# Optimization experiments

Measured on AMD Instinct MI355X. Metric: run time of the kernel, lower is better.

Reference implementation:

```python
import jax, jax.numpy as jnp
import numpy as np

N, S, D, H, L = 1024, 128, 128, 4, 2  # nodes, seq_len, d_model(=heads*C), heads, layers
C = D // H
EPS = 1e-5


def _bn(x, g, b):
    # torch BatchNorm1d training mode applied to [N, D, S]: per-channel stats over (node, seq)
    m = x.mean(axis=(0, 1))
    v = x.var(axis=(0, 1))  # biased variance, matching torch BN normalization
    return (x - m) * jax.lax.rsqrt(v + EPS) * g + b


def _ln(x, g, b):
    m = x.mean(-1, keepdims=True)
    v = x.var(-1, keepdims=True)
    return (x - m) * jax.lax.rsqrt(v + EPS) * g + b


def setup_inputs() -> dict:
    key = jax.random.key(0)
    ks = jax.random.split(key, 16)
    w = lambda k, shape: (jax.random.normal(k, shape, jnp.float32) * 0.05)
    x = jax.random.normal(ks[0], (N, S, D), jnp.float32)
    pad_mask = (jax.random.uniform(ks[1], (N, S, S)) > 0.2).astype(jnp.float32)
    ones = lambda shape: jnp.ones(shape, jnp.float32)
    zeros = lambda shape: jnp.zeros(shape, jnp.float32)
    inp = {
        'x': x, 'pad_mask': pad_mask,
        'lin_in_W': w(ks[2], (D, D)), 'lin_in_b': zeros((D,)),
        'in_bn_g': ones((D,)), 'in_bn_b': zeros((D,)),
        'q_W': w(ks[3], (L, D, D)), 'q_b': zeros((L, D)),
        'q_bn_g': ones((L, D)), 'q_bn_b': zeros((L, D)),
        'k_W': w(ks[4], (L, D, D)), 'k_b': zeros((L, D)),
        'k_bn_g': ones((L, D)), 'k_bn_b': zeros((L, D)),
        'v_W': w(ks[5], (L, D, D)), 'v_b': zeros((L, D)),
        'v_bn_g': ones((L, D)), 'v_bn_b': zeros((L, D)),
        'ln_g': ones((L, D)), 'ln_b': zeros((L, D)),
        'ff_W': w(ks[6], (L, D, D)), 'ff_b': zeros((L, D)),
        'ff_bn_g': ones((L, D)), 'ff_bn_b': zeros((L, D)),
        'skip_W': w(ks[7], (L, D, D)), 'skip_b': zeros((L, D)),
        'skip_bn_g': ones((L, D)), 'skip_bn_b': zeros((L, D)),
    }
    return inp


def reference(x, pad_mask, lin_in_W, lin_in_b, in_bn_g, in_bn_b,
              q_W, q_b, q_bn_g, q_bn_b, k_W, k_b, k_bn_g, k_bn_b,
              v_W, v_b, v_bn_g, v_bn_b, ln_g, ln_b,
              ff_W, ff_b, ff_bn_g, ff_bn_b, skip_W, skip_b, skip_bn_g, skip_bn_b):
    # DetourTransformer.forward: lin_in -> in_bn -> L DetourTransformerLayers -> take seq position 0
    h = _bn(x @ lin_in_W.T + lin_in_b, in_bn_g, in_bn_b)
    mask = pad_mask[:, None]  # [N,1,S,S], multiplicative mask applied BEFORE softmax
    for l in range(L):
        q = _bn(h @ q_W[l].T + q_b[l], q_bn_g[l], q_bn_b[l]).reshape(N, S, H, C)
        k = _bn(h @ k_W[l].T + k_b[l], k_bn_g[l], k_bn_b[l]).reshape(N, S, H, C)
        v = _bn(h @ v_W[l].T + v_b[l], v_bn_g[l], v_bn_b[l]).reshape(N, S, H, C)
        alpha = jnp.einsum('nshc,nthc->nhst', q, k) * mask  # no 1/sqrt(C) scaling in source
        attn = jax.nn.softmax(alpha, axis=-1)
        agg = jnp.einsum('nhst,nthc->nshc', attn, v).reshape(N, S, D)  # concat=True
        out = _ln(agg + h, ln_g[l], ln_b[l])
        ff = _bn(out @ ff_W[l].T + ff_b[l], ff_bn_g[l], ff_bn_b[l])
        out = _ln(out + ff, ln_g[l], ln_b[l])  # same shared LayerNorm params reused
        x_r = _bn(h @ skip_W[l].T + skip_b[l], skip_bn_g[l], skip_bn_b[l])
        h = out + x_r  # root_weight=True, beta=False
    return h[:, 0]
```

## Files before the change

kernel.cpp:

```cpp
#include <hip/hip_runtime.h>
#include <hip/hip_bf16.h>


typedef __attribute__((ext_vector_type(8))) short short8v;
typedef __attribute__((ext_vector_type(16))) float f32x16;

#define NBATCH 1024
#define SEQ    128
#define DIM    128
#define NLAYER 2
#define MTOT   (NBATCH*SEQ)
#define EPSF   1e-5f
#define INV_M  (1.0f/131072.0f)
#define HM32   ((long)MTOT * 32)
#define WMAT   16384

__device__ __forceinline__ float bf2f(ushort s) {
  return __uint_as_float(((uint)s) << 16);
}
__device__ __forceinline__ ushort f2bf(float f) {
  uint u = __float_as_uint(f);
  return (ushort)((u + 0x7FFFu + ((u >> 16) & 1u)) >> 16);
}
__device__ __forceinline__ void bfsplit(float x, short& h, short& l) {
  ushort hu = f2bf(x);
  h = (short)hu;
  l = (short)f2bf(x - bf2f(hu));
}

struct WPtrs { const float* p[11]; };

__global__ __launch_bounds__(256) void prep_w(
    WPtrs wp, ushort* __restrict__ dhi, ushort* __restrict__ dlo)
{
  const int gid = blockIdx.x * 256 + threadIdx.x;
  const int m = gid >> 11;
  const int rem = gid & 2047;
  const int j = rem >> 4, kc = rem & 15;
  const float* src = wp.p[m];
  float4 a = *(const float4*)(src + j * DIM + kc * 8);
  float4 b = *(const float4*)(src + j * DIM + kc * 8 + 4);
  float xs[8] = {a.x, a.y, a.z, a.w, b.x, b.y, b.z, b.w};
  short8v vh, vl;
#pragma unroll
  for (int i = 0; i < 8; ++i) { short h, l; bfsplit(xs[i], h, l); vh[i] = h; vl[i] = l; }
  const int nt = j >> 5, ln = j & 31;
  const int idx = m * WMAT + kc * 1024 + nt * 256 + ln * 8;
  *(short8v*)(dhi + idx) = vh;
  *(short8v*)(dlo + idx) = vl;
}

__global__ __launch_bounds__(256) void pack_mask(
    const float* __restrict__ mask, uint4* __restrict__ mb)
{
  const int lane = threadIdx.x & 63;
  const int wv   = (blockIdx.x * 256 + threadIdx.x) >> 6;
  const int NW   = gridDim.x * 4;
  for (int row = wv; row < MTOT; row += NW) {
    const float a = mask[(long)row * SEQ + lane];
    const float b = mask[(long)row * SEQ + 64 + lane];
    const unsigned long long lo = __ballot(a != 0.f);
    const unsigned long long hi = __ballot(b != 0.f);
    if (lane == 0) {
      uint4 w;
      w.x = (uint)lo; w.y = (uint)(lo >> 32);
      w.z = (uint)hi; w.w = (uint)(hi >> 32);
      mb[row] = w;
    }
  }
}

template<int OM>
__global__ __launch_bounds__(256) void gemm_one(
    const float* __restrict__ A,
    const ushort* __restrict__ Whi, const ushort* __restrict__ Wlo,
    void* __restrict__ outp, float* __restrict__ stats)
{
  __shared__ ushort Wh[16384];
  __shared__ ushort Wl[16384];
  __shared__ float tb[4][512];
  const int tid = threadIdx.x;
  const int lane = tid & 63, wid = tid >> 6;
  const int hi = lane >> 5, ln = lane & 31;
  const long m0 = (long)blockIdx.x * 128;
  const long arow = m0 + wid * 32 + ln;

#pragma unroll
  for (int i = 0; i < 8; ++i) {
    ((short8v*)Wh)[i * 256 + tid] = ((const short8v*)Whi)[i * 256 + tid];
    ((short8v*)Wl)[i * 256 + tid] = ((const short8v*)Wlo)[i * 256 + tid];
  }

  short8v ahi[8], alo[8];
  {
    const float* ar = A + arow * DIM + hi * 8;
#pragma unroll
    for (int kt = 0; kt < 8; ++kt) {
      float4 a0 = *(const float4*)(ar + kt * 16);
      float4 a1 = *(const float4*)(ar + kt * 16 + 4);
      float xs[8] = {a0.x, a0.y, a0.z, a0.w, a1.x, a1.y, a1.z, a1.w};
      short8v vh, vl;
#pragma unroll
      for (int i = 0; i < 8; ++i) { short h, l; bfsplit(xs[i], h, l); vh[i] = h; vl[i] = l; }
      ahi[kt] = vh; alo[kt] = vl;
    }
  }
  __syncthreads();

  f32x16 acc[4];
#pragma unroll
  for (int nt = 0; nt < 4; ++nt)
#pragma unroll
    for (int r = 0; r < 16; ++r) acc[nt][r] = 0.f;

#pragma unroll
  for (int kt = 0; kt < 8; ++kt) {
    const int co = (kt * 2 + hi) * 1024 + ln * 8;
#pragma unroll
    for (int nt = 0; nt < 4; ++nt) {
      short8v bh = *(const short8v*)(Wh + co + nt * 256);
      short8v bl = *(const short8v*)(Wl + co + nt * 256);
      acc[nt] = __builtin_amdgcn_mfma_f32_32x32x16_bf16(ahi[kt], bh, acc[nt], 0, 0, 0);
      acc[nt] = __builtin_amdgcn_mfma_f32_32x32x16_bf16(alo[kt], bh, acc[nt], 0, 0, 0);
      acc[nt] = __builtin_amdgcn_mfma_f32_32x32x16_bf16(ahi[kt], bl, acc[nt], 0, 0, 0);
    }
  }

  float ps[4], pq[4];
#pragma unroll
  for (int nt = 0; nt < 4; ++nt) { ps[nt] = 0.f; pq[nt] = 0.f; }

  if constexpr (OM == 0) {
#pragma unroll
    for (int nt = 0; nt < 4; ++nt) {
#pragma unroll
      for (int h2 = 0; h2 < 2; ++h2) {
#pragma unroll
        for (int rr = 0; rr < 8; ++rr) {
          const int r = h2 * 8 + rr;
          const float v = acc[nt][r];
          ps[nt] += v; pq[nt] += v * v;
          const int lrow = (rr & 3) + 8 * (rr >> 2) + 4 * hi;
          tb[wid][lrow * 32 + ln] = v;
        }
#pragma unroll
        for (int i = 0; i < 2; ++i) {
          const int lrow = i * 8 + (lane >> 3);
          float4 v = *(const float4*)&tb[wid][lrow * 32 + (lane & 7) * 4];
          *(float4*)((float*)outp + (m0 + wid * 32 + h2 * 16 + lrow) * DIM + nt * 32 + (lane & 7) * 4) = v;
        }
      }
    }
  } else {
    ushort* utb = (ushort*)&tb[wid][0];
#pragma unroll
    for (int nt = 0; nt < 4; ++nt) {
#pragma unroll
      for (int r = 0; r < 16; ++r) {
        const float v = acc[nt][r];
        ps[nt] += v; pq[nt] += v * v;
        const int row = (r & 3) + 8 * (r >> 2) + 4 * hi;
        utb[row * 32 + ln] = f2bf(v);
      }
      ushort* dst = (ushort*)outp + (long)nt * HM32 + (m0 + wid * 32) * 32;
      short8v v0 = *(const short8v*)&utb[lane * 8];
      short8v v1 = *(const short8v*)&utb[512 + lane * 8];
      *(short8v*)(dst + lane * 8)       = v0;
      *(short8v*)(dst + 512 + lane * 8) = v1;
    }
  }

#pragma unroll
  for (int nt = 0; nt < 4; ++nt) {
    ps[nt] += __shfl_xor(ps[nt], 32);
    pq[nt] += __shfl_xor(pq[nt], 32);
  }
  float* cs = (float*)tb;
  __syncthreads();
  if (tid < 256) cs[tid] = 0.f;
  __syncthreads();
  if (hi == 0) {
#pragma unroll
    for (int nt = 0; nt < 4; ++nt) {
      atomicAdd(&cs[nt * 32 + ln], ps[nt]);
      atomicAdd(&cs[128 + nt * 32 + ln], pq[nt]);
    }
  }
  __syncthreads();
  if (tid < 128) {
    atomicAdd(&stats[tid],       cs[tid]);
    atomicAdd(&stats[128 + tid], cs[128 + tid]);
  }
}

__global__ __launch_bounds__(256) void gemm_qkvs(
    const float* __restrict__ A,
    const ushort* __restrict__ whi, const ushort* __restrict__ wlo,
    ushort* __restrict__ o0, ushort* __restrict__ o1,
    ushort* __restrict__ o2, ushort* __restrict__ o3,
    float* __restrict__ st0, float* __restrict__ st1,
    float* __restrict__ st2, float* __restrict__ st3)
{
  __shared__ ushort wbuf[2][16384];
  __shared__ ushort qtb[4][1024];
  __shared__ float cs2[1024];
  const int tid = threadIdx.x;
  const int lane = tid & 63, wid = tid >> 6;
  const int hi = lane >> 5, ln = lane & 31;
  const long m0 = (long)blockIdx.x * 128;
  const long arow = m0 + wid * 32 + ln;

  short8v ahi[8], alo[8];
  {
    const float* ar = A + arow * DIM + hi * 8;
#pragma unroll
    for (int kt = 0; kt < 8; ++kt) {
      float4 a0 = *(const float4*)(ar + kt * 16);
      float4 a1 = *(const float4*)(ar + kt * 16 + 4);
      float xs[8] = {a0.x, a0.y, a0.z, a0.w, a1.x, a1.y, a1.z, a1.w};
      short8v vh, vl;
#pragma unroll
      for (int i = 0; i < 8; ++i) { short h, l; bfsplit(xs[i], h, l); vh[i] = h; vl[i] = l; }
      ahi[kt] = vh; alo[kt] = vl;
    }
  }

  {
    const short8v* sh = (const short8v*)(whi);
    const short8v* sl = (const short8v*)(wlo);
    short8v* d = (short8v*)wbuf[0];
#pragma unroll
    for (int i = 0; i < 4; ++i) d[i * 256 + tid] = sh[i * 256 + tid];
#pragma unroll
    for (int i = 0; i < 4; ++i) d[1024 + i * 256 + tid] = sl[i * 256 + tid];
    cs2[tid] = 0.f; cs2[256 + tid] = 0.f; cs2[512 + tid] = 0.f; cs2[768 + tid] = 0.f;
  }

  f32x16 acc[4];
  __syncthreads();

#pragma unroll
  for (int s = 0; s < 8; ++s) {
    const int w = s >> 1, half = s & 1;
    constexpr int wofl[4] = {0, 1, 2, 4};

    short8v nw[8];
    if (s < 7) {
      const int ns = s + 1;
      const int off = wofl[ns >> 1] * WMAT + (ns & 1) * 8192;
      const short8v* sh = (const short8v*)(whi + off);
      const short8v* sl = (const short8v*)(wlo + off);
#pragma unroll
      for (int i = 0; i < 4; ++i) nw[i] = sh[i * 256 + tid];
#pragma unroll
      for (int i = 0; i < 4; ++i) nw[4 + i] = sl[i * 256 + tid];
    }

    if (half == 0) {
#pragma unroll
      for (int nt = 0; nt < 4; ++nt)
#pragma unroll
        for (int r = 0; r < 16; ++r) acc[nt][r] = 0.f;
    }

    const ushort* wt = wbuf[s & 1];
#pragma unroll
    for (int ktl = 0; ktl < 4; ++ktl) {
      const int kt = half * 4 + ktl;
      const int co = (ktl * 2 + hi) * 1024 + ln * 8;
#pragma unroll
      for (int nt = 0; nt < 4; ++nt) {
        short8v bh = *(const short8v*)(wt + co + nt * 256);
        short8v bl = *(const short8v*)(wt + 8192 + co + nt * 256);
        acc[nt] = __builtin_amdgcn_mfma_f32_32x32x16_bf16(ahi[kt], bh, acc[nt], 0, 0, 0);
        acc[nt] = __builtin_amdgcn_mfma_f32_32x32x16_bf16(alo[kt], bh, acc[nt], 0, 0, 0);
        acc[nt] = __builtin_amdgcn_mfma_f32_32x32x16_bf16(ahi[kt], bl, acc[nt], 0, 0, 0);
      }
    }

    if (s < 7) {
      short8v* d = (short8v*)wbuf[(s + 1) & 1];
#pragma unroll
      for (int i = 0; i < 4; ++i) d[i * 256 + tid] = nw[i];
#pragma unroll
      for (int i = 0; i < 4; ++i) d[1024 + i * 256 + tid] = nw[4 + i];
    }

    if (half == 1) {
      ushort* outp = (w == 0) ? o0 : (w == 1) ? o1 : (w == 2) ? o2 : o3;
      float lps[4], lpq[4];
#pragma unroll
      for (int nt = 0; nt < 4; ++nt) { lps[nt] = 0.f; lpq[nt] = 0.f; }
#pragma unroll
      for (int nt = 0; nt < 4; ++nt) {
#pragma unroll
        for (int r = 0; r < 16; ++r) {
          const float v = acc[nt][r];
          lps[nt] += v; lpq[nt] += v * v;
          const int row = (r & 3) + 8 * (r >> 2) + 4 * hi;
          qtb[wid][row * 32 + ln] = f2bf(v);
        }
        ushort* dst = outp + (long)nt * HM32 + (m0 + wid * 32) * 32;
        short8v v0 = *(const short8v*)&qtb[wid][lane * 8];
        short8v v1 = *(const short8v*)&qtb[wid][512 + lane * 8];
        *(short8v*)(dst + lane * 8)       = v0;
        *(short8v*)(dst + 512 + lane * 8) = v1;
      }
#pragma unroll
      for (int nt = 0; nt < 4; ++nt) {
        lps[nt] += __shfl_xor(lps[nt], 32);
        lpq[nt] += __shfl_xor(lpq[nt], 32);
      }
      if (hi == 0) {
#pragma unroll
        for (int nt = 0; nt < 4; ++nt) {
          atomicAdd(&cs2[w * 256 + nt * 32 + ln], lps[nt]);
          atomicAdd(&cs2[w * 256 + 128 + nt * 32 + ln], lpq[nt]);
        }
      }
    }
    __syncthreads();
  }

  if (tid < 128) {
    atomicAdd(&st0[tid],       cs2[tid]);
    atomicAdd(&st0[128 + tid], cs2[128 + tid]);
    atomicAdd(&st1[tid],       cs2[256 + tid]);
    atomicAdd(&st1[128 + tid], cs2[384 + tid]);
    atomicAdd(&st2[tid],       cs2[512 + tid]);
    atomicAdd(&st2[128 + tid], cs2[640 + tid]);
    atomicAdd(&st3[tid],       cs2[768 + tid]);
    atomicAdd(&st3[128 + tid], cs2[896 + tid]);
  }
}

__global__ __launch_bounds__(256) void bn_apply(
    float* __restrict__ x, const float* __restrict__ st,
    const float* __restrict__ g, const float* __restrict__ b)
{
  __shared__ float sc[128], bi[128];
  const int tid = threadIdx.x;
  if (tid < 128) {
    float mean = st[tid] * INV_M;
    float var  = st[128 + tid] * INV_M - mean * mean;
    float s = rsqrtf(var + EPSF) * g[tid];
    sc[tid] = s;
    bi[tid] = b[tid] - mean * s;
  }
  __syncthreads();
  const long total4 = (long)MTOT * DIM / 4;
  for (long i = (long)blockIdx.x * 256 + tid; i < total4; i += (long)gridDim.x * 256) {
    float4 vv = ((const float4*)x)[i];
    const int c = (int)((i * 4) & 127);
    vv.x = vv.x * sc[c + 0] + bi[c + 0];
    vv.y = vv.y * sc[c + 1] + bi[c + 1];
    vv.z = vv.z * sc[c + 2] + bi[c + 2];
    vv.w = vv.w * sc[c + 3] + bi[c + 3];
    ((float4*)x)[i] = vv;
  }
}

__global__ __launch_bounds__(256) void attn_ln(
    const ushort* __restrict__ q, const ushort* __restrict__ k_in,
    const ushort* __restrict__ v_in,
    float* hbuf,
    const uint4* __restrict__ mb,
    const float* __restrict__ qst, const float* __restrict__ kst, const float* __restrict__ vst,
    const float* __restrict__ qg, const float* __restrict__ qbb,
    const float* __restrict__ kg, const float* __restrict__ kbb,
    const float* __restrict__ vg, const float* __restrict__ vbb,
    const float* __restrict__ lng, const float* __restrict__ lnb)
{
  __shared__ ushort Vp[128 * 136];
  __shared__ float qsc[128], qbi[128], ksc[128], kbi[128];
  __shared__ float reds[32][4], redq[32][4];
  __shared__ float2 rmv[32];

  const int tid = threadIdx.x;
  const int lane = tid & 63, hh = tid >> 6;
  const int hi = lane >> 5, ln = lane & 31;
  const int n = blockIdx.x;
  const long nb = (long)n * SEQ;
  const long hbase = (long)hh * HM32 + nb * 32;

  if (tid < 128) {
    const int c = tid;
    float m, v, s;
    m = qst[c] * INV_M; v = qst[128 + c] * INV_M - m * m;
    s = rsqrtf(v + EPSF) * qg[c];  qsc[c] = s; qbi[c] = qbb[c] - m * s;
    m = kst[c] * INV_M; v = kst[128 + c] * INV_M - m * m;
    s = rsqrtf(v + EPSF) * kg[c];  ksc[c] = s; kbi[c] = kbb[c] - m * s;
  }
  const int cg = hh * 32 + ln;
  float vs, vb0;
  {
    float m = vst[cg] * INV_M;
    float v = vst[128 + cg] * INV_M - m * m;
    vs = rsqrtf(v + EPSF) * vg[cg];
    vb0 = vbb[cg] - m * vs;
  }
  const float lgc = lng[cg], lbc = lnb[cg];

#pragma unroll
  for (int it = 0; it < 8; ++it) {
    const int t = it * 16 + (lane >> 2);
    const int c0 = (lane & 3) * 8;
    short8v vv = *(const short8v*)(v_in + hbase + (long)t * 32 + c0);
    const int tl = t & 31;
    const int kt = tl >> 4;
    const int rem = tl & 15;
    const int slot = (t & 96) + (kt << 4) + ((rem >> 2) & 1) * 8 + ((rem & 3) | (((rem >> 3) & 1) << 2));
#pragma unroll
    for (int i = 0; i < 8; ++i) Vp[(hh * 32 + c0 + i) * 136 + slot] = (ushort)vv[i];
  }
  __syncthreads();

  short8v kfr[4][2];
#pragma unroll
  for (int nt = 0; nt < 4; ++nt)
#pragma unroll
    for (int kt = 0; kt < 2; ++kt) {
      short8v raw = *(const short8v*)(k_in + hbase + (long)(nt * 32 + ln) * 32 + kt * 16 + hi * 8);
      short8v f;
#pragma unroll
      for (int i = 0; i < 8; ++i) {
        const int c = hh * 32 + kt * 16 + hi * 8 + i;
        f[i] = (short)f2bf(bf2f((ushort)raw[i]) * ksc[c] + kbi[c]);
      }
      kfr[nt][kt] = f;
    }

  for (int mt = 0; mt < 4; ++mt) {
    short8v qfr[2];
#pragma unroll
    for (int kt = 0; kt < 2; ++kt) {
      short8v raw = *(const short8v*)(q + hbase + (long)(mt * 32 + ln) * 32 + kt * 16 + hi * 8);
      short8v f;
#pragma unroll
      for (int i = 0; i < 8; ++i) {
        const int c = hh * 32 + kt * 16 + hi * 8 + i;
        f[i] = (short)f2bf(bf2f((ushort)raw[i]) * qsc[c] + qbi[c]);
      }
      qfr[kt] = f;
    }

    f32x16 st[4];
#pragma unroll
    for (int nt = 0; nt < 4; ++nt)
#pragma unroll
      for (int r = 0; r < 16; ++r) st[nt][r] = 0.f;
#pragma unroll
    for (int nt = 0; nt < 4; ++nt) {
      st[nt] = __builtin_amdgcn_mfma_f32_32x32x16_bf16(kfr[nt][0], qfr[0], st[nt], 0, 0, 0);
      st[nt] = __builtin_amdgcn_mfma_f32_32x32x16_bf16(kfr[nt][1], qfr[1], st[nt], 0, 0, 0);
    }

    const uint4 bw = mb[nb + mt * 32 + ln];
    float mx = -1e30f;
#pragma unroll
    for (int nt = 0; nt < 4; ++nt) {
      const uint word = (nt == 0) ? bw.x : (nt == 1) ? bw.y : (nt == 2) ? bw.z : bw.w;
#pragma unroll
      for (int r = 0; r < 16; ++r) {
        const int crow = (r & 3) + 8 * (r >> 2) + 4 * hi;
        st[nt][r] = ((word >> crow) & 1u) ? st[nt][r] : 0.f;
        mx = fmaxf(mx, st[nt][r]);
      }
    }
    mx = fmaxf(mx, __shfl_xor(mx, 32));
    float sum = 0.f;
#pragma unroll
    for (int nt = 0; nt < 4; ++nt)
#pragma unroll
      for (int r = 0; r < 16; ++r) {
        const float e = __expf(st[nt][r] - mx);
        st[nt][r] = e;
        sum += e;
      }
    sum += __shfl_xor(sum, 32);
    const float inv = 1.f / sum;

    f32x16 o;
#pragma unroll
    for (int r = 0; r < 16; ++r) o[r] = 0.f;
#pragma unroll
    for (int nt = 0; nt < 4; ++nt) {
#pragma unroll
      for (int kt = 0; kt < 2; ++kt) {
        short8v phi, plo;
#pragma unroll
        for (int j = 0; j < 8; ++j) {
          short h, l; bfsplit(st[nt][kt * 8 + j] * inv, h, l);
          phi[j] = h; plo[j] = l;
        }
        short8v vb = *(const short8v*)&Vp[(long)cg * 136 + nt * 32 + kt * 16 + hi * 8];
        o = __builtin_amdgcn_mfma_f32_32x32x16_bf16(phi, vb, o, 0, 0, 0);
        o = __builtin_amdgcn_mfma_f32_32x32x16_bf16(plo, vb, o, 0, 0, 0);
      }
    }

    float yv[16];
#pragma unroll
    for (int r = 0; r < 16; ++r) {
      const int sl = (r & 3) + 8 * (r >> 2) + 4 * hi;
      const float hval = hbuf[(nb + mt * 32 + sl) * DIM + cg];
      yv[r] = vs * o[r] + vb0 + hval;
    }

#pragma unroll
    for (int r = 0; r < 16; ++r) {
      float s = yv[r], q2 = yv[r] * yv[r];
      s += __shfl_xor(s, 1);  q2 += __shfl_xor(q2, 1);
      s += __shfl_xor(s, 2);  q2 += __shfl_xor(q2, 2);
      s += __shfl_xor(s, 4);  q2 += __shfl_xor(q2, 4);
      s += __shfl_xor(s, 8);  q2 += __shfl_xor(q2, 8);
      s += __shfl_xor(s, 16); q2 += __shfl_xor(q2, 16);
      if (ln == 0) {
        const int sl = (r & 3) + 8 * (r >> 2) + 4 * hi;
        reds[sl][hh] = s; redq[sl][hh] = q2;
      }
    }
    __syncthreads();
    if (tid < 32) {
      const float s  = reds[tid][0] + reds[tid][1] + reds[tid][2] + reds[tid][3];
      const float q2 = redq[tid][0] + redq[tid][1] + redq[tid][2] + redq[tid][3];
      const float mean = s * (1.f / 128.f);
      const float var  = q2 * (1.f / 128.f) - mean * mean;
      rmv[tid] = make_float2(mean, rsqrtf(var + EPSF));
    }
    __syncthreads();
#pragma unroll
    for (int r = 0; r < 16; ++r) {
      const int sl = (r & 3) + 8 * (r >> 2) + 4 * hi;
      const float2 mr = rmv[sl];
      hbuf[(nb + mt * 32 + sl) * DIM + cg] = (yv[r] - mr.x) * mr.y * lgc + lbc;
    }
  }
}

template <bool FINAL>
__global__ __launch_bounds__(256) void fuse2_k(
    const float* t1, const ushort* __restrict__ ffr, const ushort* __restrict__ skr,
    const float* __restrict__ fst, const float* __restrict__ sst,
    const float* __restrict__ fg, const float* __restrict__ fb,
    const float* __restrict__ sg, const float* __restrict__ sb,
    const float* __restrict__ lg, const float* __restrict__ lb,
    float* out)
{
  const int lane = threadIdx.x & 63;
  const int c = lane * 2;
  float fs0, fbias0, fs1, fbias1, ss0, sbias0, ss1, sbias1;
  {
    float m0 = fst[c] * INV_M;
    float v0 = fst[128 + c] * INV_M - m0 * m0;
    fs0 = rsqrtf(v0 + EPSF) * fg[c];       fbias0 = fb[c] - m0 * fs0;
    float m1 = fst[c + 1] * INV_M;
    float v1 = fst[128 + c + 1] * INV_M - m1 * m1;
    fs1 = rsqrtf(v1 + EPSF) * fg[c + 1];   fbias1 = fb[c + 1] - m1 * fs1;
    float n0 = sst[c] * INV_M;
    float w0 = sst[128 + c] * INV_M - n0 * n0;
    ss0 = rsqrtf(w0 + EPSF) * sg[c];       sbias0 = sb[c] - n0 * ss0;
    float n1 = sst[c + 1] * INV_M;
    float w1 = sst[128 + c + 1] * INV_M - n1 * n1;
    ss1 = rsqrtf(w1 + EPSF) * sg[c + 1];   sbias1 = sb[c + 1] - n1 * ss1;
  }
  const float lg0 = lg[c], lg1 = lg[c + 1], lb0 = lb[c], lb1 = lb[c + 1];
  const int wid = (blockIdx.x * 256 + threadIdx.x) >> 6;
  const int NW  = gridDim.x * 4;
  const int ROWS = FINAL ? NBATCH : MTOT;
  const long thm = (long)(c >> 5) * HM32;
  for (int r = wid; r < ROWS; r += NW) {
    const long m   = FINAL ? (long)r * SEQ : (long)r;
    const long off = m * DIM + c;
    const long hm  = thm + m * 32 + (c & 31);
    float2 tv = *(const float2*)(t1 + off);
    uint fv = *(const uint*)(ffr + hm);
    uint sv = *(const uint*)(skr + hm);
    float f0 = bf2f((ushort)(fv & 0xFFFFu)), f1 = bf2f((ushort)(fv >> 16));
    float s0 = bf2f((ushort)(sv & 0xFFFFu)), s1 = bf2f((ushort)(sv >> 16));
    float y0 = tv.x + f0 * fs0 + fbias0;
    float y1 = tv.y + f1 * fs1 + fbias1;
    float s = y0 + y1, sq = y0 * y0 + y1 * y1;
#pragma unroll
    for (int o = 32; o; o >>= 1) { s += __shfl_xor(s, o); sq += __shfl_xor(sq, o); }
    const float mean = s * (1.f / 128.f);
    const float var  = sq * (1.f / 128.f) - mean * mean;
    const float rs   = rsqrtf(var + EPSF);
    float o0 = (y0 - mean) * rs * lg0 + lb0 + (s0 * ss0 + sbias0);
    float o1 = (y1 - mean) * rs * lg1 + lb1 + (s1 * ss1 + sbias1);
    const long ooff = FINAL ? ((long)r * DIM + c) : off;
    *(float2*)(out + ooff) = make_float2(o0, o1);
  }
}

extern "C" void kernel_launch(void* const* d_in, const int* in_sizes, int n_in,
                              void* d_out, int out_size, void* d_ws, size_t ws_size,
                              hipStream_t stream)
{
  (void)in_sizes; (void)n_in; (void)out_size; (void)ws_size;
  const float* x    = (const float*)d_in[0];
  const float* mask = (const float*)d_in[1];
  const float* linW = (const float*)d_in[2];
  const float* ing  = (const float*)d_in[4];
  const float* inb  = (const float*)d_in[5];
  const float* qW   = (const float*)d_in[6];
  const float* qg   = (const float*)d_in[8];
  const float* qb   = (const float*)d_in[9];
  const float* kW   = (const float*)d_in[10];
  const float* kg   = (const float*)d_in[12];
  const float* kb   = (const float*)d_in[13];
  const float* vW   = (const float*)d_in[14];
  const float* vg   = (const float*)d_in[16];
  const float* vb   = (const float*)d_in[17];
  const float* lng  = (const float*)d_in[18];
  const float* lnb  = (const float*)d_in[19];
  const float* ffW  = (const float*)d_in[20];
  const float* ffg  = (const float*)d_in[22];
  const float* ffb  = (const float*)d_in[23];
  const float* skW  = (const float*)d_in[24];
  const float* skg  = (const float*)d_in[26];
  const float* skb  = (const float*)d_in[27];

  const long MD = (long)MTOT * DIM;
  float*  stats = (float*)d_ws;
  ushort* whi   = (ushort*)((char*)d_ws + 16384);
  ushort* wlo   = whi + 11 * WMAT;
  float*  h     = (float*)(wlo + 11 * WMAT);
  ushort* qbuf  = (ushort*)(h + MD);
  ushort* kbuf  = qbuf + MD;
  ushort* vbuf  = kbuf + MD;
  ushort* sbuf  = vbuf + MD;
  uint4*  mbits = (uint4*)(sbuf + MD);
  ushort* ffbuf = qbuf;

  hipMemsetAsync(stats, 0, 11 * 256 * sizeof(float), stream);

  WPtrs wp;
  wp.p[0] = linW;
  wp.p[1] = qW;            wp.p[2] = kW;            wp.p[3] = vW;
  wp.p[4] = ffW;           wp.p[5] = skW;
  wp.p[6] = qW + 16384;    wp.p[7] = kW + 16384;    wp.p[8] = vW + 16384;
  wp.p[9] = ffW + 16384;   wp.p[10] = skW + 16384;
  prep_w<<<88, 256, 0, stream>>>(wp, whi, wlo);
  pack_mask<<<512, 256, 0, stream>>>(mask, mbits);

  gemm_one<0><<<MTOT / 128, 256, 0, stream>>>(x, whi, wlo, h, stats);
  bn_apply<<<1024, 256, 0, stream>>>(h, stats, ing, inb);

  for (int l = 0; l < NLAYER; ++l) {
    const int poff = l * DIM;
    const int wbase = (1 + 5 * l) * WMAT;
    float* stq = stats + (1 + 5 * l) * 256;
    float* stk = stats + (2 + 5 * l) * 256;
    float* stv = stats + (3 + 5 * l) * 256;
    float* stf = stats + (4 + 5 * l) * 256;
    float* sts = stats + (5 + 5 * l) * 256;

    gemm_qkvs<<<MTOT / 128, 256, 0, stream>>>(h, whi + wbase, wlo + wbase,
                                              qbuf, kbuf, vbuf, sbuf,
                                              stq, stk, stv, sts);

    attn_ln<<<NBATCH, 256, 0, stream>>>(
        qbuf, kbuf, vbuf, h , mbits,
        stq, stk, stv,
        qg + poff, qb + poff, kg + poff, kb + poff, vg + poff, vb + poff,
        lng + poff, lnb + poff);

    gemm_one<2><<<MTOT / 128, 256, 0, stream>>>(
        h, whi + wbase + 3 * WMAT, wlo + wbase + 3 * WMAT, ffbuf, stf);

    if (l < NLAYER - 1) {
      fuse2_k<false><<<1024, 256, 0, stream>>>(
          h, ffbuf, sbuf, stf, sts,
          ffg + poff, ffb + poff, skg + poff, skb + poff,
          lng + poff, lnb + poff, h );
    } else {
      fuse2_k<true><<<64, 256, 0, stream>>>(
          h, ffbuf, sbuf, stf, sts,
          ffg + poff, ffb + poff, skg + poff, skb + poff,
          lng + poff, lnb + poff, (float*)d_out);
    }
  }
}
```

Baseline: 580.8 us.

## Fold input BatchNorm into consumer kernels and deepen weight prefetch

Removes the standalone bn_apply pass over h after the input projection. Layer-0 gemm_qkvs and attn_ln now apply the input BN scale and bias on the fly from the stats, which saves one full read-write sweep of the fp32 activation. It also changes the weight prefetch in gemm_qkvs to load two stages ahead using alternating register buffers, at some cost in register pressure. Because attn_ln writes h in place, the normalized values are presumably materialised there for later consumers.

```diff
diff --git a/kernel.cpp b/kernel.cpp
--- a/kernel.cpp
+++ b/kernel.cpp
@@ -193,22 +193,56 @@
   }
 }
 
+template<bool BN>
 __global__ __launch_bounds__(256) void gemm_qkvs(
     const float* __restrict__ A,
     const ushort* __restrict__ whi, const ushort* __restrict__ wlo,
     ushort* __restrict__ o0, ushort* __restrict__ o1,
     ushort* __restrict__ o2, ushort* __restrict__ o3,
     float* __restrict__ st0, float* __restrict__ st1,
-    float* __restrict__ st2, float* __restrict__ st3)
+    float* __restrict__ st2, float* __restrict__ st3,
+    const float* __restrict__ bnst, const float* __restrict__ bng,
+    const float* __restrict__ bnb)
 {
   __shared__ ushort wbuf[2][16384];
   __shared__ ushort qtb[4][1024];
   __shared__ float cs2[1024];
+  __shared__ float hscb[256];
   const int tid = threadIdx.x;
   const int lane = tid & 63, wid = tid >> 6;
   const int hi = lane >> 5, ln = lane & 31;
   const long m0 = (long)blockIdx.x * 128;
   const long arow = m0 + wid * 32 + ln;
+  constexpr int wofl[4] = {0, 1, 2, 4};
+
+  {
+    const short8v* sh = (const short8v*)(whi);
+    const short8v* sl = (const short8v*)(wlo);
+    short8v* d = (short8v*)wbuf[0];
+#pragma unroll
+    for (int i = 0; i < 4; ++i) d[i * 256 + tid] = sh[i * 256 + tid];
+#pragma unroll
+    for (int i = 0; i < 4; ++i) d[1024 + i * 256 + tid] = sl[i * 256 + tid];
+    if constexpr (BN) {
+      if (tid < 128) {
+        const float m = bnst[tid] * INV_M;
+        const float v = bnst[128 + tid] * INV_M - m * m;
+        const float s = rsqrtf(v + EPSF) * bng[tid];
+        hscb[tid] = s;
+        hscb[128 + tid] = bnb[tid] - m * s;
+      }
+    }
+    cs2[tid] = 0.f; cs2[256 + tid] = 0.f; cs2[512 + tid] = 0.f; cs2[768 + tid] = 0.f;
+  }
+
+  short8v nwA[8], nwB[8];
+  {
+    const short8v* sh = (const short8v*)(whi + 8192);
+    const short8v* sl = (const short8v*)(wlo + 8192);
+#pragma unroll
+    for (int i = 0; i < 4; ++i) { nwA[i] = sh[i * 256 + tid]; nwA[4 + i] = sl[i * 256 + tid]; }
+  }
+  __syncthreads();
 
   short8v ahi[8], alo[8];
   {
@@ -220,40 +254,36 @@
       float xs[8] = {a0.x, a0.y, a0.z, a0.w, a1.x, a1.y, a1.z, a1.w};
       short8v vh, vl;
 #pragma unroll
-      for (int i = 0; i < 8; ++i) { short h, l; bfsplit(xs[i], h, l); vh[i] = h; vl[i] = l; }
+      for (int i = 0; i < 8; ++i) {
+        float x = xs[i];
+        if constexpr (BN) {
+          const int c = kt * 16 + hi * 8 + i;
+          x = x * hscb[c] + hscb[128 + c];
+        }
+        short h, l; bfsplit(x, h, l); vh[i] = h; vl[i] = l;
+      }
       ahi[kt] = vh; alo[kt] = vl;
     }
   }
 
-  {
-    const short8v* sh = (const short8v*)(whi);
-    const short8v* sl = (const short8v*)(wlo);
-    short8v* d = (short8v*)wbuf[0];
-#pragma unroll
-    for (int i = 0; i < 4; ++i) d[i * 256 + tid] = sh[i * 256 + tid];
-#pragma unroll
-    for (int i = 0; i < 4; ++i) d[1024 + i * 256 + tid] = sl[i * 256 + tid];
-    cs2[tid] = 0.f; cs2[256 + tid] = 0.f; cs2[512 + tid] = 0.f; cs2[768 + tid] = 0.f;
-  }
-
   f32x16 acc[4];
-  __syncthreads();
 
 #pragma unroll
   for (int s = 0; s < 8; ++s) {
     const int w = s >> 1, half = s & 1;
-    constexpr int wofl[4] = {0, 1, 2, 4};
-
-    short8v nw[8];
-    if (s < 7) {
-      const int ns = s + 1;
+
+    if (s < 6) {
+      const int ns = s + 2;
       const int off = wofl[ns >> 1] * WMAT + (ns & 1) * 8192;
       const short8v* sh = (const short8v*)(whi + off);
       const short8v* sl = (const short8v*)(wlo + off);
-#pragma unroll
-      for (int i = 0; i < 4; ++i) nw[i] = sh[i * 256 + tid];
-#pragma unroll
-      for (int i = 0; i < 4; ++i) nw[4 + i] = sl[i * 256 + tid];
+      if (s & 1) {
+#pragma unroll
+        for (int i = 0; i < 4; ++i) { nwA[i] = sh[i * 256 + tid]; nwA[4 + i] = sl[i * 256 + tid]; }
+      } else {
+#pragma unroll
+        for (int i = 0; i < 4; ++i) { nwB[i] = sh[i * 256 + tid]; nwB[4 + i] = sl[i * 256 + tid]; }
+      }
     }
 
     if (half == 0) {
@@ -280,10 +310,13 @@
 
     if (s < 7) {
       short8v* d = (short8v*)wbuf[(s + 1) & 1];
-#pragma unroll
-      for (int i = 0; i < 4; ++i) d[i * 256 + tid] = nw[i];
-#pragma unroll
-      for (int i = 0; i < 4; ++i) d[1024 + i * 256 + tid] = nw[4 + i];
+      if (s & 1) {
+#pragma unroll
+        for (int i = 0; i < 4; ++i) { d[i * 256 + tid] = nwB[i]; d[1024 + i * 256 + tid] = nwB[4 + i]; }
+      } else {
+#pragma unroll
+        for (int i = 0; i < 4; ++i) { d[i * 256 + tid] = nwA[i]; d[1024 + i * 256 + tid] = nwA[4 + i]; }
+      }
     }
 
     if (half == 1) {
@@ -334,32 +367,6 @@
   }
 }
 
-__global__ __launch_bounds__(256) void bn_apply(
-    float* __restrict__ x, const float* __restrict__ st,
-    const float* __restrict__ g, const float* __restrict__ b)
-{
-  __shared__ float sc[128], bi[128];
-  const int tid = threadIdx.x;
-  if (tid < 128) {
-    float mean = st[tid] * INV_M;
-    float var  = st[128 + tid] * INV_M - mean * mean;
-    float s = rsqrtf(var + EPSF) * g[tid];
-    sc[tid] = s;
-    bi[tid] = b[tid] - mean * s;
-  }
-  __syncthreads();
-  const long total4 = (long)MTOT * DIM / 4;
-  for (long i = (long)blockIdx.x * 256 + tid; i < total4; i += (long)gridDim.x * 256) {
-    float4 vv = ((const float4*)x)[i];
-    const int c = (int)((i * 4) & 127);
-    vv.x = vv.x * sc[c + 0] + bi[c + 0];
-    vv.y = vv.y * sc[c + 1] + bi[c + 1];
-    vv.z = vv.z * sc[c + 2] + bi[c + 2];
-    vv.w = vv.w * sc[c + 3] + bi[c + 3];
-    ((float4*)x)[i] = vv;
-  }
-}
-
 __global__ __launch_bounds__(256) void attn_ln(
     const ushort* __restrict__ q, const ushort* __restrict__ k_in,
     const ushort* __restrict__ v_in,
@@ -369,7 +376,9 @@
     const float* __restrict__ qg, const float* __restrict__ qbb,
     const float* __restrict__ kg, const float* __restrict__ kbb,
     const float* __restrict__ vg, const float* __restrict__ vbb,
-    const float* __restrict__ lng, const float* __restrict__ lnb)
+    const float* __restrict__ lng, const float* __restrict__ lnb,
+    const float* __restrict__ hstp, const float* __restrict__ hgp,
+    const float* __restrict__ hbp)
 {
   __shared__ ushort Vp[128 * 136];
   __shared__ float qsc[128], qbi[128], ksc[128], kbi[128];
@@ -400,6 +409,13 @@
     vb0 = vbb[cg] - m * vs;
   }
   const float lgc = lng[cg], lbc = lnb[cg];
+  float hsc = 1.f, hbi2 = 0.f;
+  if (hstp) {
+    const float m = hstp[cg] * INV_M;
+    const float v = hstp[128 + cg] * INV_M - m * m;
+    const float s = rsqrtf(v + EPSF) * hgp[cg];
+    hsc = s; hbi2 = hbp[cg] - m * s;
+  }
 
 #pragma unroll
   for (int it = 0; it < 8; ++it) {
@@ -504,7 +520,7 @@
     for (int r = 0; r < 16; ++r) {
       const int sl = (r & 3) + 8 * (r >> 2) + 4 * hi;
       const float hval = hbuf[(nb + mt * 32 + sl) * DIM + cg];
-      yv[r] = vs * o[r] + vb0 + hval;
+      yv[r] = vs * o[r] + vb0 + (hval * hsc + hbi2);
     }
 
 #pragma unroll
@@ -645,7 +661,6 @@
   pack_mask<<<512, 256, 0, stream>>>(mask, mbits);
 
   gemm_one<0><<<MTOT / 128, 256, 0, stream>>>(x, whi, wlo, h, stats);
-  bn_apply<<<1024, 256, 0, stream>>>(h, stats, ing, inb);
 
   for (int l = 0; l < NLAYER; ++l) {
     const int poff = l * DIM;
@@ -656,15 +671,23 @@
     float* stf = stats + (4 + 5 * l) * 256;
     float* sts = stats + (5 + 5 * l) * 256;
 
-    gemm_qkvs<<<MTOT / 128, 256, 0, stream>>>(h, whi + wbase, wlo + wbase,
-                                              qbuf, kbuf, vbuf, sbuf,
-                                              stq, stk, stv, sts);
-
-    attn_ln<<<NBATCH, 256, 0, stream>>>(
-        qbuf, kbuf, vbuf, h , mbits,
-        stq, stk, stv,
-        qg + poff, qb + poff, kg + poff, kb + poff, vg + poff, vb + poff,
-        lng + poff, lnb + poff);
+    if (l == 0) {
+      gemm_qkvs<true><<<MTOT / 128, 256, 0, stream>>>(
+          h, whi + wbase, wlo + wbase, qbuf, kbuf, vbuf, sbuf,
+          stq, stk, stv, sts, stats, ing, inb);
+      attn_ln<<<NBATCH, 256, 0, stream>>>(
+          qbuf, kbuf, vbuf, h, mbits, stq, stk, stv,
+          qg + poff, qb + poff, kg + poff, kb + poff, vg + poff, vb + poff,
+          lng + poff, lnb + poff, stats, ing, inb);
+    } else {
+      gemm_qkvs<false><<<MTOT / 128, 256, 0, stream>>>(
+          h, whi + wbase, wlo + wbase, qbuf, kbuf, vbuf, sbuf,
+          stq, stk, stv, sts, nullptr, nullptr, nullptr);
+      attn_ln<<<NBATCH, 256, 0, stream>>>(
+          qbuf, kbuf, vbuf, h, mbits, stq, stk, stv,
+          qg + poff, qb + poff, kg + poff, kb + poff, vg + poff, vb + poff,
+          lng + poff, lnb + poff, nullptr, nullptr, nullptr);
+    }
 
     gemm_one<2><<<MTOT / 128, 256, 0, stream>>>(
         h, whi + wbase + 3 * WMAT, wlo + wbase + 3 * WMAT, ffbuf, stf);
```

New measurement: 618.3 us. 1.06x slower.
